# Kernel optimization log

Measured on AMD Instinct MI355X. Metric: run time of the kernel, lower is better.

## Reference

```python
import jax, jax.numpy as jnp
import numpy as np
import math

B, T, D_MOTION = 2, 1536, 256
D_MODEL, N_HEADS, D_FF, N_LAYERS = 512, 8, 2048, 6
D_HEAD = D_MODEL // N_HEADS
FPS = 30
PERIOD = FPS // 2
CONTEXT_FRAMES = 10
NEG = -1e9  # large negative instead of -inf so fully-masked rows give uniform attn, not NaN


def _w(k, shape, fan_in):
    return jax.random.normal(k, shape, jnp.float32) / np.sqrt(fan_in)


def setup_inputs() -> dict:
    key = jax.random.key(0)
    ks = jax.random.split(key, 16)
    L = N_LAYERS
    din = D_MOTION + 5 + 1
    inp = {
        'motion': jax.random.normal(ks[0], (B, T, D_MOTION), jnp.float32),
        'traj': jax.random.normal(ks[1], (B, T, 5), jnp.float32),
        'me_w1': _w(ks[2], (din, D_MODEL), din), 'me_b1': jnp.zeros((D_MODEL,), jnp.float32),
        'me_w2': _w(ks[3], (D_MODEL, D_MODEL), D_MODEL), 'me_b2': jnp.zeros((D_MODEL,), jnp.float32),
        'wq': _w(ks[4], (L, D_MODEL, D_MODEL), D_MODEL), 'bq': jnp.zeros((L, D_MODEL), jnp.float32),
        'wk': _w(ks[5], (L, D_MODEL, D_MODEL), D_MODEL), 'bk': jnp.zeros((L, D_MODEL), jnp.float32),
        'wv': _w(ks[6], (L, D_MODEL, D_MODEL), D_MODEL), 'bv': jnp.zeros((L, D_MODEL), jnp.float32),
        'wo': _w(ks[7], (L, D_MODEL, D_MODEL), D_MODEL), 'bo': jnp.zeros((L, D_MODEL), jnp.float32),
        'ln1_g': jnp.ones((L, D_MODEL), jnp.float32), 'ln1_b': jnp.zeros((L, D_MODEL), jnp.float32),
        'ffn_w1': _w(ks[8], (L, D_MODEL, D_FF), D_MODEL), 'ffn_b1': jnp.zeros((L, D_FF), jnp.float32),
        'ffn_w2': _w(ks[9], (L, D_FF, D_MODEL), D_FF), 'ffn_b2': jnp.zeros((L, D_MODEL), jnp.float32),
        'ln2_g': jnp.ones((L, D_MODEL), jnp.float32), 'ln2_b': jnp.zeros((L, D_MODEL), jnp.float32),
        'fln_g': jnp.ones((D_MODEL,), jnp.float32), 'fln_b': jnp.zeros((D_MODEL,), jnp.float32),
        'dec_w1': _w(ks[10], (D_MODEL, D_MODEL), D_MODEL), 'dec_b1': jnp.zeros((D_MODEL,), jnp.float32),
        'dec_w2': _w(ks[11], (D_MODEL, D_MOTION), D_MODEL), 'dec_b2': jnp.zeros((D_MOTION,), jnp.float32),
    }
    return inp


def _layer_norm(x, g, b):
    m = jnp.mean(x, axis=-1, keepdims=True)
    v = jnp.mean((x - m) ** 2, axis=-1, keepdims=True)
    return (x - m) * jax.lax.rsqrt(v + 1e-5) * g + b


def _leaky(x):
    return jnp.where(x >= 0, x, 0.01 * x)


def _forward(motion, traj, me_w1, me_b1, me_w2, me_b2, wq, bq, wk, bk, wv, bv, wo, bo,
             ln1_g, ln1_b, ffn_w1, ffn_b1, ffn_w2, ffn_b2, ln2_g, ln2_b,
             fln_g, fln_b, dec_w1, dec_b1, dec_w2, dec_b2):
    idx = jnp.arange(T)
    dist = jnp.abs(idx[:, None] - idx[None, :])                       # [T,T]
    atten_bias = -(dist // PERIOD).astype(jnp.float32)                # periodic distance bias

    # context mask: keep first context_frames and last frame
    batch_mask = jnp.ones((T, 1), jnp.float32).at[CONTEXT_FRAMES:-1].set(0.0)
    mask = jnp.broadcast_to(batch_mask[None], (B, T, 1))              # [B,T,1]
    cf = jnp.ones((T,), bool).at[CONTEXT_FRAMES:-1].set(False)        # constrained frames

    original_motion = motion
    motion = motion * mask

    # motion encoder (dropout inactive at eval)
    h = jnp.concatenate([motion, traj, mask], axis=-1)                # [B,T,D_MOTION+6]
    x = _leaky(h @ me_w1 + me_b1)
    x = _leaky(x @ me_w2 + me_b2)

    # periodic positional embedding (sinusoidal on pos mod period)
    pos = jnp.mod(jnp.arange(T, dtype=jnp.float32), float(PERIOD))
    half = D_MODEL // 2
    div = jnp.exp(-np.log(10000.0) * (2.0 * jnp.arange(half, dtype=jnp.float32)) / D_MODEL)
    ang = pos[:, None] * div[None, :]
    pe = jnp.concatenate([jnp.sin(ang), jnp.cos(ang)], axis=-1)       # [T,D_MODEL]
    x = x + pe[None]

    # dynamically growing attention window
    num_trans = T - CONTEXT_FRAMES - 1
    ksz = math.ceil(num_trans / 2 / N_LAYERS) * 2 + 1
    kern = jnp.ones((ksz,), jnp.float32)
    thr = ksz // 2
    scale = 1.0 / np.sqrt(D_HEAD)

    for i in range(N_LAYERS):
        # attn mask: True = blocked
        amask = (dist > thr) | (~cf)[None, :]                         # [T,T]
        h = _layer_norm(x, ln1_g[i], ln1_b[i])                        # pre-layernorm
        q = (h @ wq[i] + bq[i]).reshape(B, T, N_HEADS, D_HEAD)
        k = (h @ wk[i] + bk[i]).reshape(B, T, N_HEADS, D_HEAD)
        v = (h @ wv[i] + bv[i]).reshape(B, T, N_HEADS, D_HEAD)
        scores = jnp.einsum('bqhd,bkhd->bhqk', q, k) * scale + atten_bias
        scores = jnp.where(amask[None, None], NEG, scores)
        attn = jax.nn.softmax(scores, axis=-1)
        out = jnp.einsum('bhqk,bkhd->bqhd', attn, v).reshape(B, T, D_MODEL)
        x = x + out @ wo[i] + bo[i]
        # position-wise FFN (pre-layernorm)
        h = _layer_norm(x, ln2_g[i], ln2_b[i])
        x = x + jax.nn.relu(h @ ffn_w1[i] + ffn_b1[i]) @ ffn_w2[i] + ffn_b2[i]
        # grow constrained frames by conv1d with ones kernel (same padding)
        cf = jnp.convolve(cf.astype(jnp.float32), kern, mode='same') > 0.5

    x = _layer_norm(x, fln_g, fln_b)
    x = _leaky(x @ dec_w1 + dec_b1)
    x = x @ dec_w2 + dec_b2                                           # [B,T,D_MOTION]
    out = original_motion * mask + x * (1.0 - mask)
    return out, mask


def reference(motion, traj, me_w1, me_b1, me_w2, me_b2, wq, bq, wk, bk, wv, bv, wo, bo,
              ln1_g, ln1_b, ffn_w1, ffn_b1, ffn_w2, ffn_b2, ln2_g, ln2_b,
              fln_g, fln_b, dec_w1, dec_b1, dec_w2, dec_b2):
    return _forward(motion, traj, me_w1, me_b1, me_w2, me_b2, wq, bq, wk, bk, wv, bv, wo, bo,
                    ln1_g, ln1_b, ffn_w1, ffn_b1, ffn_w2, ffn_b2, ln2_g, ln2_b,
                    fln_g, fln_b, dec_w1, dec_b1, dec_w2, dec_b2)
```

## Files before the change

kernel.cpp:

```cpp
#include <hip/hip_runtime.h>
#include <math.h>

typedef unsigned short ushort_t;
typedef unsigned int uint_t;
typedef __bf16 bf16x4 __attribute__((ext_vector_type(4)));
typedef __bf16 bf16x8 __attribute__((ext_vector_type(8)));
typedef float f32x4 __attribute__((ext_vector_type(4)));

#define T_SEQ   1536
#define NB      2
#define MROWS   3072
#define DMODEL  512
#define NHEADS  8
#define DHEAD   64
#define DFF     2048
#define DMOTION 256
#define NLAYERS 6
#define PERIODN 15
#define CTXF    10
#define THRW    128
#define KIN     384

__device__ __forceinline__ float bf2f(ushort_t u) { return __uint_as_float((uint_t)u << 16); }
__device__ __forceinline__ ushort_t f2bf(float f) {
    uint_t x = __float_as_uint(f);
    return (ushort_t)((x + 0x7fffu + ((x >> 16) & 1u)) >> 16);
}

__device__ __forceinline__ void gl2lds(const ushort_t* g, ushort_t* l) {
    __builtin_amdgcn_global_load_lds((const __attribute__((address_space(1))) void*)g,
                                     (__attribute__((address_space(3))) void*)l, 16, 0, 0);
}

__global__ __launch_bounds__(256) void pe_k(float* __restrict__ pe) {
    int idx = blockIdx.x * 256 + threadIdx.x;
    if (idx >= PERIODN * DMODEL) return;
    int p = idx / DMODEL, c = idx % DMODEL;
    int j = (c < DMODEL / 2) ? c : (c - DMODEL / 2);
    float div = __expf(-logf(10000.0f) * (2.0f * (float)j) / (float)DMODEL);
    float ang = (float)p * div;
    pe[idx] = (c < DMODEL / 2) ? sinf(ang) : cosf(ang);
}

__global__ __launch_bounds__(256) void build_k(const float* __restrict__ motion,
                                               const float* __restrict__ traj,
                                               ushort_t* __restrict__ hin,
                                               float* __restrict__ mask_out) {
    int idx = blockIdx.x * 256 + threadIdx.x;
    if (idx >= MROWS * KIN) return;
    int row = idx / KIN, c = idx % KIN;
    int t = row % T_SEQ;
    float mv = (t < CTXF || t == T_SEQ - 1) ? 1.0f : 0.0f;
    float val;
    if (c < DMOTION)            val = motion[(size_t)row * DMOTION + c] * mv;
    else if (c < DMOTION + 5)   val = traj[(size_t)row * 5 + (c - DMOTION)];
    else if (c == DMOTION + 5)  val = mv;
    else                        val = 0.0f;
    hin[idx] = f2bf(val);
    if (c == 0) mask_out[row] = mv;
}

__global__ __launch_bounds__(256)
void tconv_k(const float* __restrict__ src, size_t sstride,
             ushort_t* __restrict__ dst, size_t dstride,
             int K, int N, int Kpad) {
    __shared__ float t[32][33];
    src += (size_t)blockIdx.z * sstride;
    dst += (size_t)blockIdx.z * dstride;
    const int kb = blockIdx.y * 32, nb = blockIdx.x * 32;
    const int tx = threadIdx.x & 31, ty = threadIdx.x >> 5;
#pragma unroll
    for (int i = 0; i < 4; ++i) {
        int k = kb + ty + i * 8, n = nb + tx;
        t[ty + i * 8][tx] = (k < K && n < N) ? src[(size_t)k * N + n] : 0.0f;
    }
    __syncthreads();
#pragma unroll
    for (int i = 0; i < 4; ++i) {
        int n = nb + ty + i * 8, kk = kb + tx;
        if (n < N && kk < Kpad) dst[(size_t)n * Kpad + kk] = f2bf(t[tx][ty + i * 8]);
    }
}

__global__ __launch_bounds__(256)
void tconv_qkv_k(const float* __restrict__ wq, const float* __restrict__ wk,
                 const float* __restrict__ wv, ushort_t* __restrict__ qkvt) {
    __shared__ float t[32][33];
    const int z = blockIdx.z, s = z % 3, l = z / 3;
    const float* src = (s == 0 ? wq : s == 1 ? wk : wv) + (size_t)l * DMODEL * DMODEL;
    ushort_t* dst = qkvt + (size_t)z * DMODEL * DMODEL;
    const int kb = blockIdx.y * 32, nb = blockIdx.x * 32;
    const int tx = threadIdx.x & 31, ty = threadIdx.x >> 5;
#pragma unroll
    for (int i = 0; i < 4; ++i)
        t[ty + i * 8][tx] = src[(size_t)(kb + ty + i * 8) * DMODEL + nb + tx];
    __syncthreads();
#pragma unroll
    for (int i = 0; i < 4; ++i)
        dst[(size_t)(nb + ty + i * 8) * DMODEL + kb + tx] = f2bf(t[tx][ty + i * 8]);
}

__global__ __launch_bounds__(256)
void bcat_k(const float* __restrict__ bq, const float* __restrict__ bk,
            const float* __restrict__ bv, float* __restrict__ bqkv) {
    int idx = blockIdx.x * 256 + threadIdx.x;
    if (idx >= NLAYERS * 3 * DMODEL) return;
    int l = idx / (3 * DMODEL), n = idx % (3 * DMODEL);
    int s = n >> 9, c = n & 511;
    const float* b = (s == 0 ? bq : s == 1 ? bk : bv);
    bqkv[idx] = b[l * DMODEL + c];
}

#define CL  68
template <int ACT, bool RES, bool PE, bool OUTBF>
__global__ __launch_bounds__(256)
void qgemm_k(const ushort_t* __restrict__ A, int K,
             const ushort_t* __restrict__ Wt,
             const float* __restrict__ bias,
             const float* __restrict__ res,
             const float* __restrict__ pe15,
             void* __restrict__ Cout, int N) {
    __shared__ ushort_t smem[2][(32 + 64) * 128];
    const int tid = threadIdx.x;
    const int lane = tid & 63, wid = tid >> 6;
    const int m0 = blockIdx.y * 32, n0 = blockIdx.x * 64;
    const int l4 = lane >> 4, l15 = lane & 15;
    const int lrow = lane >> 4;
    const int lu   = lane & 15;

    f32x4 acc[2][4];
#pragma unroll
    for (int m = 0; m < 2; ++m)
#pragma unroll
        for (int n = 0; n < 4; ++n) acc[m][n] = (f32x4){0.f, 0.f, 0.f, 0.f};

    const int niter = K >> 7;

    auto stage = [&](int buf, int k0) {
        ushort_t* dst = &smem[buf][0];
#pragma unroll
        for (int j = 0; j < 6; ++j) {
            const int inst = wid * 6 + j;
            if (inst < 8) {
                const int row = inst * 4 + lrow;
                const int u = lu ^ (row & 15);
                gl2lds(A + (size_t)(m0 + row) * K + k0 + u * 8, dst + inst * 512);
            } else {
                const int bi = inst - 8;
                const int row = bi * 4 + lrow;
                const int u = lu ^ (row & 15);
                gl2lds(Wt + (size_t)(n0 + row) * K + k0 + u * 8,
                       dst + 32 * 128 + bi * 512);
            }
        }
    };

    const int kbyte = wid * 64;
    auto rdfrag = [&](const ushort_t* t, int row) -> bf16x8 {
        const int off0 = kbyte + l4 * 8;
        const int off1 = kbyte + 32 + l4 * 8;
        const int a0 = row * 256 + (((off0 & ~15) ^ ((row & 15) << 4)) | (off0 & 15));
        const int a1 = row * 256 + (((off1 & ~15) ^ ((row & 15) << 4)) | (off1 & 15));
        bf16x4 lo = *(const bf16x4*)((const char*)t + a0);
        bf16x4 hi = *(const bf16x4*)((const char*)t + a1);
        return __builtin_shufflevector(lo, hi, 0, 1, 2, 3, 4, 5, 6, 7);
    };

    stage(0, 0);
    __syncthreads();
    int cur = 0;
    for (int t = 0; t < niter; ++t) {
        if (t + 1 < niter) stage(cur ^ 1, (t + 1) << 7);
        const ushort_t* As = &smem[cur][0];
        const ushort_t* Bs = &smem[cur][32 * 128];
        bf16x8 af[2], bf[4];
#pragma unroll
        for (int m = 0; m < 2; ++m) af[m] = rdfrag(As, m * 16 + l15);
#pragma unroll
        for (int n = 0; n < 4; ++n) bf[n] = rdfrag(Bs, n * 16 + l15);
#pragma unroll
        for (int m = 0; m < 2; ++m)
#pragma unroll
            for (int n = 0; n < 4; ++n)
                acc[m][n] = __builtin_amdgcn_mfma_f32_16x16x32_bf16(af[m], bf[n], acc[m][n], 0, 0, 0);
        __syncthreads();
        cur ^= 1;
    }

    float* cb0 = (float*)&smem[0][0];
    float* cb1 = (float*)&smem[1][0];
    if (wid >= 2) {
        float* cb = (wid == 2) ? cb0 : cb1;
#pragma unroll
        for (int m = 0; m < 2; ++m)
#pragma unroll
            for (int n = 0; n < 4; ++n)
#pragma unroll
                for (int r = 0; r < 4; ++r)
                    cb[(m * 16 + l4 * 4 + r) * CL + n * 16 + l15] = acc[m][n][r];
    }
    __syncthreads();
    if (wid < 2) {
        float* cb = (wid == 0) ? cb0 : cb1;
#pragma unroll
        for (int m = 0; m < 2; ++m)
#pragma unroll
            for (int n = 0; n < 4; ++n)
#pragma unroll
                for (int r = 0; r < 4; ++r)
                    cb[(m * 16 + l4 * 4 + r) * CL + n * 16 + l15] += acc[m][n][r];
    }
    __syncthreads();

    const int row = tid >> 3, c0 = (tid & 7) * 8;
    const int grow = m0 + row;
#pragma unroll
    for (int j = 0; j < 8; ++j) {
        const int gcol = n0 + c0 + j;
        float v = cb0[row * CL + c0 + j] + cb1[row * CL + c0 + j] + bias[gcol];
        if (ACT == 1) v = v >= 0.f ? v : 0.01f * v;
        else if (ACT == 2) v = fmaxf(v, 0.f);
        else if (ACT == 3) {
            const int t2 = grow % T_SEQ;
            const float mv = (t2 < CTXF || t2 == T_SEQ - 1) ? 1.0f : 0.0f;
            v = res[(size_t)grow * N + gcol] * mv + v * (1.0f - mv);
        }
        if (PE) v += pe15[((grow % T_SEQ) % PERIODN) * DMODEL + gcol];
        if (RES) v += res[(size_t)grow * N + gcol];
        if (OUTBF) ((ushort_t*)Cout)[(size_t)grow * N + gcol] = f2bf(v);
        else       ((float*)Cout)[(size_t)grow * N + gcol] = v;
    }
}

template <bool RES, bool OUTBF>
__global__ __launch_bounds__(256)
void pgemm_k(const ushort_t* __restrict__ A,
             const ushort_t* __restrict__ Wt,
             const float* __restrict__ bias,
             const float* __restrict__ res,
             void* __restrict__ Cout, int ldc,
             int tpb, int len1, int start2, int nact) {
    __shared__ ushort_t smem[2][(32 + 64) * 128];
    const int tid = threadIdx.x;
    const int lane = tid & 63, wid = tid >> 6;
    const int ty = blockIdx.y;
    const int bb = (ty >= tpb) ? 1 : 0;
    const int t32 = (ty - bb * tpb) * 32;
    const int n0 = blockIdx.x * 64;
    const int l4 = lane >> 4, l15 = lane & 15;
    const int lrow = lane >> 4;
    const int lu   = lane & 15;

    auto maprow = [&](int pr) -> size_t {
        int r = t32 + pr;
        r = min(r, nact - 1);
        int tt = (r < len1) ? r : (start2 + (r - len1));
        return (size_t)(bb * T_SEQ + tt);
    };

    f32x4 acc[2][4];
#pragma unroll
    for (int m = 0; m < 2; ++m)
#pragma unroll
        for (int n = 0; n < 4; ++n) acc[m][n] = (f32x4){0.f, 0.f, 0.f, 0.f};

    auto stage = [&](int buf, int k0) {
        ushort_t* dst = &smem[buf][0];
#pragma unroll
        for (int j = 0; j < 6; ++j) {
            const int inst = wid * 6 + j;
            if (inst < 8) {
                const int row = inst * 4 + lrow;
                const int u = lu ^ (row & 15);
                gl2lds(A + maprow(row) * 512 + k0 + u * 8, dst + inst * 512);
            } else {
                const int bi = inst - 8;
                const int row = bi * 4 + lrow;
                const int u = lu ^ (row & 15);
                gl2lds(Wt + (size_t)(n0 + row) * 512 + k0 + u * 8,
                       dst + 32 * 128 + bi * 512);
            }
        }
    };

    const int kbyte = wid * 64;
    auto rdfrag = [&](const ushort_t* t, int row) -> bf16x8 {
        const int off0 = kbyte + l4 * 8;
        const int off1 = kbyte + 32 + l4 * 8;
        const int a0 = row * 256 + (((off0 & ~15) ^ ((row & 15) << 4)) | (off0 & 15));
        const int a1 = row * 256 + (((off1 & ~15) ^ ((row & 15) << 4)) | (off1 & 15));
        bf16x4 lo = *(const bf16x4*)((const char*)t + a0);
        bf16x4 hi = *(const bf16x4*)((const char*)t + a1);
        return __builtin_shufflevector(lo, hi, 0, 1, 2, 3, 4, 5, 6, 7);
    };

    stage(0, 0);
    __syncthreads();
    int cur = 0;
    for (int t = 0; t < 4; ++t) {
        if (t + 1 < 4) stage(cur ^ 1, (t + 1) << 7);
        const ushort_t* As = &smem[cur][0];
        const ushort_t* Bs = &smem[cur][32 * 128];
        bf16x8 af[2], bf[4];
#pragma unroll
        for (int m = 0; m < 2; ++m) af[m] = rdfrag(As, m * 16 + l15);
#pragma unroll
        for (int n = 0; n < 4; ++n) bf[n] = rdfrag(Bs, n * 16 + l15);
#pragma unroll
        for (int m = 0; m < 2; ++m)
#pragma unroll
            for (int n = 0; n < 4; ++n)
                acc[m][n] = __builtin_amdgcn_mfma_f32_16x16x32_bf16(af[m], bf[n], acc[m][n], 0, 0, 0);
        __syncthreads();
        cur ^= 1;
    }

    float* cb0 = (float*)&smem[0][0];
    float* cb1 = (float*)&smem[1][0];
    if (wid >= 2) {
        float* cb = (wid == 2) ? cb0 : cb1;
#pragma unroll
        for (int m = 0; m < 2; ++m)
#pragma unroll
            for (int n = 0; n < 4; ++n)
#pragma unroll
                for (int r = 0; r < 4; ++r)
                    cb[(m * 16 + l4 * 4 + r) * CL + n * 16 + l15] = acc[m][n][r];
    }
    __syncthreads();
    if (wid < 2) {
        float* cb = (wid == 0) ? cb0 : cb1;
#pragma unroll
        for (int m = 0; m < 2; ++m)
#pragma unroll
            for (int n = 0; n < 4; ++n)
#pragma unroll
                for (int r = 0; r < 4; ++r)
                    cb[(m * 16 + l4 * 4 + r) * CL + n * 16 + l15] += acc[m][n][r];
    }
    __syncthreads();

    const int row = tid >> 3, c0 = (tid & 7) * 8;
    const int pr = t32 + row;
    if (pr >= nact) return;
    const int tt = (pr < len1) ? pr : (start2 + (pr - len1));
    const size_t grow = (size_t)(bb * T_SEQ + tt);
#pragma unroll
    for (int j = 0; j < 8; ++j) {
        const int gcol = n0 + c0 + j;
        float v = cb0[row * CL + c0 + j] + cb1[row * CL + c0 + j] + bias[gcol];
        if (RES) v += res[grow * ldc + gcol];
        if (OUTBF) ((ushort_t*)Cout)[grow * ldc + gcol] = f2bf(v);
        else       ((float*)Cout)[grow * ldc + gcol] = v;
    }
}

__global__ __launch_bounds__(256)
void ln_k(const float* __restrict__ X, const float* __restrict__ g,
          const float* __restrict__ b, ushort_t* __restrict__ Y) {
    const int wid = threadIdx.x >> 6, lane = threadIdx.x & 63;
    const int row = blockIdx.x * 4 + wid;
    const float* x = X + (size_t)row * DMODEL;
    float v[8], s = 0.f;
#pragma unroll
    for (int j = 0; j < 8; ++j) { v[j] = x[lane + 64 * j]; s += v[j]; }
#pragma unroll
    for (int o = 32; o; o >>= 1) s += __shfl_xor(s, o);
    const float mean = s * (1.0f / DMODEL);
    float vs = 0.f;
#pragma unroll
    for (int j = 0; j < 8; ++j) { float d = v[j] - mean; vs += d * d; }
#pragma unroll
    for (int o = 32; o; o >>= 1) vs += __shfl_xor(vs, o);
    const float inv = rsqrtf(vs * (1.0f / DMODEL) + 1e-5f);
    ushort_t* y = Y + (size_t)row * DMODEL;
#pragma unroll
    for (int j = 0; j < 8; ++j) {
        const int c = lane + 64 * j;
        y[c] = f2bf((v[j] - mean) * inv * g[c] + b[c]);
    }
}

__global__ __launch_bounds__(1024)
void vsum_k(const ushort_t* __restrict__ h, float* __restrict__ hp) {
    __shared__ float red[16][512];
    const int b = blockIdx.x, ch = blockIdx.y;
    const int rg = threadIdx.x >> 6;
    const int c8 = (threadIdx.x & 63) * 8;
    const ushort_t* hb = h + (size_t)(b * T_SEQ + ch * 192) * DMODEL + c8;
    float a[8] = {};
    for (int r = rg; r < 192; r += 16) {
        bf16x8 v = *(const bf16x8*)(hb + (size_t)r * DMODEL);
#pragma unroll
        for (int j = 0; j < 8; ++j) a[j] += (float)v[j];
    }
#pragma unroll
    for (int j = 0; j < 8; ++j) red[rg][c8 + j] = a[j];
    __syncthreads();
    if (threadIdx.x < 512) {
        float s = 0.f;
#pragma unroll
        for (int gi = 0; gi < 16; ++gi) s += red[gi][threadIdx.x];
        hp[(b * 8 + ch) * 512 + threadIdx.x] = s;
    }
}

__global__ __launch_bounds__(256)
void vdot_k(const float* __restrict__ hp, const ushort_t* __restrict__ wvt,
            const float* __restrict__ bv, float* __restrict__ vm) {
    __shared__ float mh[512];
    __shared__ float red[256];
    const int b = blockIdx.x, seg = blockIdx.y;
    const int t = threadIdx.x;
    for (int c = t; c < 512; c += 256) {
        float s = 0.f;
#pragma unroll
        for (int ch = 0; ch < 8; ++ch) s += hp[(b * 8 + ch) * 512 + c];
        mh[c] = s * (1.0f / T_SEQ);
    }
    __syncthreads();
    const int col = seg * 128 + (t & 127);
    const int kh = (t >> 7) * 256;
    const ushort_t* w = wvt + (size_t)col * 512 + kh;
    float s = 0.f;
    for (int k = 0; k < 256; k += 8) {
        bf16x8 w8 = *(const bf16x8*)(w + k);
#pragma unroll
        for (int j = 0; j < 8; ++j) s += mh[kh + k + j] * (float)w8[j];
    }
    red[t] = s;
    __syncthreads();
    if (t < 128) vm[b * 512 + col] = red[t] + red[t + 128] + bv[col];
}

__global__ __launch_bounds__(256)
void gemv_k(const float* __restrict__ vin, const ushort_t* __restrict__ wt,
            const float* __restrict__ bias, float* __restrict__ vout) {
    __shared__ float mh[512];
    __shared__ float red[256];
    const int b = blockIdx.x, seg = blockIdx.y;
    const int t = threadIdx.x;
    for (int c = t; c < 512; c += 256) mh[c] = vin[b * 512 + c];
    __syncthreads();
    const int col = seg * 128 + (t & 127);
    const int kh = (t >> 7) * 256;
    const ushort_t* w = wt + (size_t)col * 512 + kh;
    float s = 0.f;
    for (int k = 0; k < 256; k += 8) {
        bf16x8 w8 = *(const bf16x8*)(w + k);
#pragma unroll
        for (int j = 0; j < 8; ++j) s += mh[kh + k + j] * (float)w8[j];
    }
    red[t] = s;
    __syncthreads();
    if (t < 128) vout[b * 512 + col] = red[t] + red[t + 128] + bias[col];
}

__global__ __launch_bounds__(256)
void xadd_k(const float* __restrict__ vmo, float* __restrict__ x, int q0) {
    const int row = q0 + blockIdx.x, b = blockIdx.y;
    float* xr = x + (size_t)(b * T_SEQ + row) * DMODEL;
    const float* vb = vmo + b * 512;
    xr[threadIdx.x]       += vb[threadIdx.x];
    xr[threadIdx.x + 256] += vb[threadIdx.x + 256];
}

#define KLD 72
#define VLD 36
__global__ __launch_bounds__(256)
void attn3_k(const ushort_t* __restrict__ qkv, ushort_t* __restrict__ attout,
             int lo, int hi, int nlow, int qhi0, int tl, int st) {
    __shared__ ushort_t klds_[4][32 * KLD];
    __shared__ ushort_t vlds_[4][64 * VLD];
    const int lane = threadIdx.x & 63, wid = threadIdx.x >> 6;
    const int s = blockIdx.x * 4 + wid;
    if (s >= st) return;
    const int h = blockIdx.y, b = blockIdx.z;
    const int l15 = lane & 15, l4 = lane >> 4;

    int qb, qend;
    if (s < tl) { qb = 16 * s;                qend = nlow - 1; }
    else        { qb = qhi0 + 16 * (s - tl);  qend = T_SEQ - 1; }
    const int nr = qend - qb;

    ushort_t* klds = klds_[wid];
    ushort_t* vlds = vlds_[wid];
    const size_t rbase = (size_t)(b * T_SEQ) * 1536;
    const int q = qb + l15;

    const int qrow_r = min(q, T_SEQ - 1);
    const ushort_t* qptr = qkv + rbase + (size_t)qrow_r * 1536 + h * 64;
    bf16x8 bq[2];
#pragma unroll
    for (int kh = 0; kh < 2; ++kh) {
        bf16x4 lo4 = *(const bf16x4*)(qptr + kh * 32 + l4 * 4);
        bf16x4 hi4 = *(const bf16x4*)(qptr + kh * 32 + 16 + l4 * 4);
        bq[kh] = __builtin_shufflevector(lo4, hi4, 0, 1, 2, 3, 4, 5, 6, 7);
    }

    const int band0 = max(0, qb - THRW);
    const int band1 = min(T_SEQ - 1, qb + 15 + THRW);
    const int i1s = band0, i1e = min(band1, lo - 1);
    const int i2s = max(band0, hi), i2e = band1;

    f32x4 O[4] = {{0.f,0.f,0.f,0.f},{0.f,0.f,0.f,0.f},{0.f,0.f,0.f,0.f},{0.f,0.f,0.f,0.f}};
    float m = -3.0e38f, lsum = 0.f;

#pragma unroll 1
    for (int seg = 0; seg < 2; ++seg) {
        const int s0 = seg ? i2s : i1s, s1 = seg ? i2e : i1e;
#pragma unroll 1
        for (int c0 = s0; c0 <= s1; c0 += 32) {
#pragma unroll
            for (int i = 0; i < 4; ++i) {
                const int idx = i * 64 + lane;
                const int row = idx >> 3, c = (idx & 7) * 8;
                const int kr = min(c0 + row, T_SEQ - 1);
                const uint4 kv = *(const uint4*)(qkv + rbase + (size_t)kr * 1536 + 512 + h * 64 + c);
                *(uint4*)&klds[row * KLD + c] = kv;
                const uint4 vv = *(const uint4*)(qkv + rbase + (size_t)kr * 1536 + 1024 + h * 64 + c);
                const ushort_t* vp = (const ushort_t*)&vv;
#pragma unroll
                for (int d = 0; d < 8; ++d) vlds[(c + d) * VLD + row] = vp[d];
            }
            f32x4 sacc[2];
#pragma unroll
            for (int ks = 0; ks < 2; ++ks) {
                f32x4 a = {0.f, 0.f, 0.f, 0.f};
#pragma unroll
                for (int kh = 0; kh < 2; ++kh) {
                    const ushort_t* kp = &klds[(16 * ks + l15) * KLD + kh * 32];
                    bf16x4 lo4 = *(const bf16x4*)(kp + l4 * 4);
                    bf16x4 hi4 = *(const bf16x4*)(kp + 16 + l4 * 4);
                    bf16x8 ak = __builtin_shufflevector(lo4, hi4, 0, 1, 2, 3, 4, 5, 6, 7);
                    a = __builtin_amdgcn_mfma_f32_16x16x32_bf16(ak, bq[kh], a, 0, 0, 0);
                }
                sacc[ks] = a;
            }
            float sv[8];
            bool vld[8];
            float cm = -3.0e38f;
#pragma unroll
            for (int ks = 0; ks < 2; ++ks)
#pragma unroll
                for (int r = 0; r < 4; ++r) {
                    const int key = c0 + 16 * ks + 4 * l4 + r;
                    const int dist = (q > key) ? (q - key) : (key - q);
                    const bool v = (dist <= THRW) && (key < lo || key >= hi) && (key < T_SEQ);
                    const int ii = ks * 4 + r;
                    sv[ii] = sacc[ks][r] * 0.125f - (float)(dist / PERIODN);
                    vld[ii] = v;
                    cm = fmaxf(cm, v ? sv[ii] : -3.0e38f);
                }
            cm = fmaxf(cm, __shfl_xor(cm, 16));
            cm = fmaxf(cm, __shfl_xor(cm, 32));
            const float mnew = fmaxf(m, cm);
            const float sc = __expf(m - mnew);
            m = mnew;
            float p[8], psum = 0.f;
#pragma unroll
            for (int ii = 0; ii < 8; ++ii) {
                p[ii] = vld[ii] ? __expf(sv[ii] - mnew) : 0.f;
                psum += p[ii];
            }
            psum += __shfl_xor(psum, 16);
            psum += __shfl_xor(psum, 32);
            lsum = lsum * sc + psum;
#pragma unroll
            for (int ds = 0; ds < 4; ++ds) O[ds] *= sc;
            bf16x8 pb;
#pragma unroll
            for (int ii = 0; ii < 8; ++ii) pb[ii] = (__bf16)p[ii];
#pragma unroll
            for (int ds = 0; ds < 4; ++ds) {
                const ushort_t* vp2 = &vlds[(16 * ds + l15) * VLD];
                bf16x4 lo4 = *(const bf16x4*)(vp2 + 4 * l4);
                bf16x4 hi4 = *(const bf16x4*)(vp2 + 16 + 4 * l4);
                bf16x8 av = __builtin_shufflevector(lo4, hi4, 0, 1, 2, 3, 4, 5, 6, 7);
                O[ds] = __builtin_amdgcn_mfma_f32_16x16x32_bf16(av, pb, O[ds], 0, 0, 0);
            }
        }
    }
    if (l15 <= nr) {
        const float inv = 1.0f / lsum;
        ushort_t* op = attout + (size_t)(b * T_SEQ + qb + l15) * DMODEL + h * 64;
#pragma unroll
        for (int ds = 0; ds < 4; ++ds)
#pragma unroll
            for (int r = 0; r < 4; ++r)
                op[16 * ds + 4 * l4 + r] = f2bf(O[ds][r] * inv);
    }
}

extern "C" void kernel_launch(void* const* d_in, const int* in_sizes, int n_in,
                              void* d_out, int out_size, void* d_ws, size_t ws_size,
                              hipStream_t stream) {
    const float* motion = (const float*)d_in[0];
    const float* traj   = (const float*)d_in[1];
    const float* me_w1  = (const float*)d_in[2];
    const float* me_b1  = (const float*)d_in[3];
    const float* me_w2  = (const float*)d_in[4];
    const float* me_b2  = (const float*)d_in[5];
    const float* wq = (const float*)d_in[6];
    const float* bq = (const float*)d_in[7];
    const float* wk = (const float*)d_in[8];
    const float* bk = (const float*)d_in[9];
    const float* wv = (const float*)d_in[10];
    const float* bv = (const float*)d_in[11];
    const float* wo = (const float*)d_in[12];
    const float* bo = (const float*)d_in[13];
    const float* ln1_g = (const float*)d_in[14];
    const float* ln1_b = (const float*)d_in[15];
    const float* ffn_w1 = (const float*)d_in[16];
    const float* ffn_b1 = (const float*)d_in[17];
    const float* ffn_w2 = (const float*)d_in[18];
    const float* ffn_b2 = (const float*)d_in[19];
    const float* ln2_g = (const float*)d_in[20];
    const float* ln2_b = (const float*)d_in[21];
    const float* fln_g = (const float*)d_in[22];
    const float* fln_b = (const float*)d_in[23];
    const float* dec_w1 = (const float*)d_in[24];
    const float* dec_b1 = (const float*)d_in[25];
    const float* dec_w2 = (const float*)d_in[26];
    const float* dec_b2 = (const float*)d_in[27];

    float* out = (float*)d_out;
    float* mask_out = out + (size_t)MROWS * DMOTION;

    char* base = (char*)d_ws;
    auto alloc = [&](size_t bytes) { char* p = base; base += (bytes + 255) & ~(size_t)255; return p; };

    ushort_t* qkvt  = (ushort_t*)alloc((size_t)NLAYERS * 1536 * 512 * 2);
    ushort_t* wot   = (ushort_t*)alloc((size_t)NLAYERS * 512 * 512 * 2);
    ushort_t* ffn1t = (ushort_t*)alloc((size_t)NLAYERS * 2048 * 512 * 2);
    ushort_t* ffn2t = (ushort_t*)alloc((size_t)NLAYERS * 512 * 2048 * 2);
    ushort_t* mew1t = (ushort_t*)alloc((size_t)512 * KIN * 2);
    ushort_t* mew2t = (ushort_t*)alloc((size_t)512 * 512 * 2);
    ushort_t* dec1t = (ushort_t*)alloc((size_t)512 * 512 * 2);
    ushort_t* dec2t = (ushort_t*)alloc((size_t)256 * 512 * 2);
    float*    bqkv  = (float*)alloc((size_t)NLAYERS * 1536 * 4);
    float*    pe15  = (float*)alloc((size_t)PERIODN * DMODEL * 4);
    float*    hp    = (float*)alloc((size_t)NB * 8 * 512 * 4);
    float*    vm    = (float*)alloc((size_t)NB * 512 * 4);
    float*    vmo   = (float*)alloc((size_t)NB * 512 * 4);
    ushort_t* hin   = (ushort_t*)alloc((size_t)MROWS * KIN * 2);
    float*    x     = (float*)alloc((size_t)MROWS * DMODEL * 4);
    ushort_t* h     = (ushort_t*)alloc((size_t)MROWS * DMODEL * 2);
    ushort_t* qkv   = (ushort_t*)alloc((size_t)MROWS * 1536 * 2);
    ushort_t* ff    = (ushort_t*)alloc((size_t)MROWS * DFF * 2);

    const dim3 blk(256);
    pe_k<<<(PERIODN * DMODEL + 255) / 256, blk, 0, stream>>>(pe15);
    build_k<<<(MROWS * KIN + 255) / 256, blk, 0, stream>>>(motion, traj, hin, mask_out);

    tconv_qkv_k<<<dim3(16, 16, 18), blk, 0, stream>>>(wq, wk, wv, qkvt);
    tconv_k<<<dim3(16, 16, 6), blk, 0, stream>>>(wo, 512 * 512, wot, 512 * 512, 512, 512, 512);
    tconv_k<<<dim3(64, 16, 6), blk, 0, stream>>>(ffn_w1, 512 * 2048, ffn1t, 2048 * 512, 512, 2048, 512);
    tconv_k<<<dim3(16, 64, 6), blk, 0, stream>>>(ffn_w2, 2048 * 512, ffn2t, 512 * 2048, 2048, 512, 2048);
    tconv_k<<<dim3(16, 12, 1), blk, 0, stream>>>(me_w1, 0, mew1t, 0, 262, 512, KIN);
    tconv_k<<<dim3(16, 16, 1), blk, 0, stream>>>(me_w2, 0, mew2t, 0, 512, 512, 512);
    tconv_k<<<dim3(16, 16, 1), blk, 0, stream>>>(dec_w1, 0, dec1t, 0, 512, 512, 512);
    tconv_k<<<dim3(8, 16, 1),  blk, 0, stream>>>(dec_w2, 0, dec2t, 0, 512, 256, 512);
    bcat_k<<<(NLAYERS * 1536 + 255) / 256, blk, 0, stream>>>(bq, bk, bv, bqkv);

    const dim3 gs512(8, 96), gsff(32, 96), gs256(4, 96);

    qgemm_k<1, false, false, true ><<<gs512, blk, 0, stream>>>(hin, KIN, mew1t, me_b1, nullptr, nullptr, h, 512);
    qgemm_k<1, false, true,  false><<<gs512, blk, 0, stream>>>(h, 512, mew2t, me_b2, nullptr, pe15, x, 512);

    for (int i = 0; i < NLAYERS; ++i) {
        const int lo = CTXF + THRW * i;
        const int hi = (T_SEQ - 1) - THRW * i;
        int qlow_end = lo + 127;
        int qhi0 = hi - 128;
        int nlow, ninact;
        if (qhi0 <= qlow_end + 1) {
            nlow = T_SEQ; qhi0 = T_SEQ; ninact = 0;
        } else {
            nlow = qlow_end + 1;
            ninact = qhi0 - nlow;
        }
        const int tl2 = (nlow + 15) / 16;
        const int th2 = (T_SEQ - qhi0 + 15) / 16;
        const int st  = tl2 + th2;
        const int nact_q = nlow + (T_SEQ - qhi0);
        const int tpb_q  = (nact_q + 31) / 32;
        const int nkeys  = lo + (T_SEQ - hi);
        const int tpb_kv = (nkeys + 31) / 32;

        const ushort_t* qw  = qkvt + (size_t)i * 1536 * 512;
        const ushort_t* kvw = qw + (size_t)512 * 512;
        const ushort_t* vw  = qw + (size_t)1024 * 512;
        const float* bq_i   = bqkv + i * 1536;

        ln_k<<<MROWS / 4, blk, 0, stream>>>(x, ln1_g + i * 512, ln1_b + i * 512, h);
        pgemm_k<false, true><<<dim3(8, 2 * tpb_q), blk, 0, stream>>>(
            h, qw, bq_i, nullptr, qkv, 1536, tpb_q, nlow, qhi0, nact_q);
        pgemm_k<false, true><<<dim3(16, 2 * tpb_kv), blk, 0, stream>>>(
            h, kvw, bq_i + 512, nullptr, qkv + 512, 1536, tpb_kv, lo, hi, nkeys);
        if (ninact > 0) {
            vsum_k<<<dim3(NB, 8), dim3(1024), 0, stream>>>(h, hp);
            vdot_k<<<dim3(NB, 4), blk, 0, stream>>>(hp, vw, bq_i + 1024, vm);
            gemv_k<<<dim3(NB, 4), blk, 0, stream>>>(vm, wot + (size_t)i * 512 * 512, bo + i * 512, vmo);
            xadd_k<<<dim3(ninact, NB), blk, 0, stream>>>(vmo, x, nlow);
        }
        attn3_k<<<dim3((st + 3) / 4, NHEADS, NB), blk, 0, stream>>>(qkv, h, lo, hi, nlow, qhi0, tl2, st);
        pgemm_k<true, false><<<dim3(8, 2 * tpb_q), blk, 0, stream>>>(
            h, wot + (size_t)i * 512 * 512, bo + i * 512, x, x, 512, tpb_q, nlow, qhi0, nact_q);
        ln_k<<<MROWS / 4, blk, 0, stream>>>(x, ln2_g + i * 512, ln2_b + i * 512, h);
        qgemm_k<2, false, false, true><<<gsff, blk, 0, stream>>>(h, 512, ffn1t + (size_t)i * 2048 * 512, ffn_b1 + i * 2048, nullptr, nullptr, ff, 2048);
        qgemm_k<0, true, false, false><<<gs512, blk, 0, stream>>>(ff, 2048, ffn2t + (size_t)i * 512 * 2048, ffn_b2 + i * 512, x, nullptr, x, 512);
    }

    ln_k<<<MROWS / 4, blk, 0, stream>>>(x, fln_g, fln_b, h);
    qgemm_k<1, false, false, true ><<<gs512, blk, 0, stream>>>(h, 512, dec1t, dec_b1, nullptr, nullptr, ff, 512);
    qgemm_k<3, false, false, false><<<gs256, blk, 0, stream>>>(ff, 512, dec2t, dec_b2, motion, nullptr, out, 256);
}
```

Before: 831.2 us.

## Merge weight transposes, Q/KV projections, and inactive-row vector path into fewer kernels

All weight transpose-convert launches are collapsed into one flat-grid kernel. The separate Q and KV projection GEMMs are merged into a single qkv_k launch that picks its role from blockIdx. The vdot/gemv pair becomes one 512-thread kernel, and the xadd broadcast into inactive rows is folded into the second layernorm, which adds vmo and writes x back. Together these cut launch count and one pass over x per layer, at the cost of wasted early-exit blocks in qkv_k and a larger serial gemv in a single block per batch.

```diff
diff --git a/kernel.cpp b/kernel.cpp
--- a/kernel.cpp
+++ b/kernel.cpp
@@ -61,13 +61,54 @@
 }
 
 __global__ __launch_bounds__(256)
-void tconv_k(const float* __restrict__ src, size_t sstride,
-             ushort_t* __restrict__ dst, size_t dstride,
-             int K, int N, int Kpad) {
+void tconv_all_k(const float* __restrict__ wq, const float* __restrict__ wk,
+                 const float* __restrict__ wv, const float* __restrict__ wo,
+                 const float* __restrict__ fw1, const float* __restrict__ fw2,
+                 const float* __restrict__ mw1, const float* __restrict__ mw2,
+                 const float* __restrict__ dw1, const float* __restrict__ dw2,
+                 ushort_t* __restrict__ qkvt, ushort_t* __restrict__ wot,
+                 ushort_t* __restrict__ ffn1t, ushort_t* __restrict__ ffn2t,
+                 ushort_t* __restrict__ mew1t, ushort_t* __restrict__ mew2t,
+                 ushort_t* __restrict__ dec1t, ushort_t* __restrict__ dec2t) {
     __shared__ float t[32][33];
-    src += (size_t)blockIdx.z * sstride;
-    dst += (size_t)blockIdx.z * dstride;
-    const int kb = blockIdx.y * 32, nb = blockIdx.x * 32;
+    int bid = blockIdx.x;
+    const float* src; ushort_t* dst;
+    int K, N, Kpad, kb, nb;
+    if (bid < 4608) {
+        int z = bid >> 8, r = bid & 255;
+        int s = z % 3, l = z / 3;
+        src = (s == 0 ? wq : s == 1 ? wk : wv) + (size_t)l * 262144;
+        dst = qkvt + (size_t)z * 262144;
+        K = 512; N = 512; Kpad = 512; kb = (r >> 4) * 32; nb = (r & 15) * 32;
+    } else if (bid < 6144) {
+        int b2 = bid - 4608; int z = b2 >> 8, r = b2 & 255;
+        src = wo + (size_t)z * 262144; dst = wot + (size_t)z * 262144;
+        K = 512; N = 512; Kpad = 512; kb = (r >> 4) * 32; nb = (r & 15) * 32;
+    } else if (bid < 12288) {
+        int b2 = bid - 6144; int z = b2 >> 10, r = b2 & 1023;
+        src = fw1 + (size_t)z * 1048576; dst = ffn1t + (size_t)z * 1048576;
+        K = 512; N = 2048; Kpad = 512; kb = (r >> 6) * 32; nb = (r & 63) * 32;
+    } else if (bid < 18432) {
+        int b2 = bid - 12288; int z = b2 >> 10, r = b2 & 1023;
+        src = fw2 + (size_t)z * 1048576; dst = ffn2t + (size_t)z * 1048576;
+        K = 2048; N = 512; Kpad = 2048; kb = (r >> 4) * 32; nb = (r & 15) * 32;
+    } else if (bid < 18624) {
+        int r = bid - 18432;
+        src = mw1; dst = mew1t;
+        K = 262; N = 512; Kpad = KIN; kb = (r >> 4) * 32; nb = (r & 15) * 32;
+    } else if (bid < 18880) {
+        int r = bid - 18624;
+        src = mw2; dst = mew2t;
+        K = 512; N = 512; Kpad = 512; kb = (r >> 4) * 32; nb = (r & 15) * 32;
+    } else if (bid < 19136) {
+        int r = bid - 18880;
+        src = dw1; dst = dec1t;
+        K = 512; N = 512; Kpad = 512; kb = (r >> 4) * 32; nb = (r & 15) * 32;
+    } else {
+        int r = bid - 19136;
+        src = dw2; dst = dec2t;
+        K = 512; N = 256; Kpad = 512; kb = (r >> 3) * 32; nb = (r & 7) * 32;
+    }
     const int tx = threadIdx.x & 31, ty = threadIdx.x >> 5;
 #pragma unroll
     for (int i = 0; i < 4; ++i) {
@@ -80,24 +121,6 @@
         int n = nb + ty + i * 8, kk = kb + tx;
         if (n < N && kk < Kpad) dst[(size_t)n * Kpad + kk] = f2bf(t[tx][ty + i * 8]);
     }
-}
-
-__global__ __launch_bounds__(256)
-void tconv_qkv_k(const float* __restrict__ wq, const float* __restrict__ wk,
-                 const float* __restrict__ wv, ushort_t* __restrict__ qkvt) {
-    __shared__ float t[32][33];
-    const int z = blockIdx.z, s = z % 3, l = z / 3;
-    const float* src = (s == 0 ? wq : s == 1 ? wk : wv) + (size_t)l * DMODEL * DMODEL;
-    ushort_t* dst = qkvt + (size_t)z * DMODEL * DMODEL;
-    const int kb = blockIdx.y * 32, nb = blockIdx.x * 32;
-    const int tx = threadIdx.x & 31, ty = threadIdx.x >> 5;
-#pragma unroll
-    for (int i = 0; i < 4; ++i)
-        t[ty + i * 8][tx] = src[(size_t)(kb + ty + i * 8) * DMODEL + nb + tx];
-    __syncthreads();
-#pragma unroll
-    for (int i = 0; i < 4; ++i)
-        dst[(size_t)(nb + ty + i * 8) * DMODEL + kb + tx] = f2bf(t[tx][ty + i * 8]);
 }
 
 __global__ __launch_bounds__(256)
@@ -356,6 +379,134 @@
 }
 
 __global__ __launch_bounds__(256)
+void qkv_k(const ushort_t* __restrict__ A,
+           const ushort_t* __restrict__ qw, const ushort_t* __restrict__ kvw,
+           const float* __restrict__ biasq, ushort_t* __restrict__ Cout,
+           int tpbQ, int len1Q, int start2Q, int nactQ,
+           int tpbK, int len1K, int start2K, int nactK) {
+    __shared__ ushort_t smem[2][(32 + 64) * 128];
+    const int tid = threadIdx.x;
+    const int lane = tid & 63, wid = tid >> 6;
+    int tyl, tpb, len1, start2, nact, outoff;
+    const ushort_t* W;
+    if ((int)blockIdx.y < 2 * tpbQ) {
+        if (blockIdx.x >= 8) return;
+        tyl = blockIdx.y; tpb = tpbQ; len1 = len1Q; start2 = start2Q; nact = nactQ;
+        outoff = 0; W = qw;
+    } else {
+        tyl = blockIdx.y - 2 * tpbQ; tpb = tpbK; len1 = len1K; start2 = start2K; nact = nactK;
+        outoff = 512; W = kvw;
+    }
+    const int bb = (tyl >= tpb) ? 1 : 0;
+    const int t32 = (tyl - bb * tpb) * 32;
+    const int n0 = blockIdx.x * 64;
+    const int l4 = lane >> 4, l15 = lane & 15;
+    const int lrow = lane >> 4;
+    const int lu   = lane & 15;
+
+    auto maprow = [&](int pr) -> size_t {
+        int r = t32 + pr;
+        r = min(r, nact - 1);
+        int tt = (r < len1) ? r : (start2 + (r - len1));
+        return (size_t)(bb * T_SEQ + tt);
+    };
+
+    f32x4 acc[2][4];
+#pragma unroll
+    for (int m = 0; m < 2; ++m)
+#pragma unroll
+        for (int n = 0; n < 4; ++n) acc[m][n] = (f32x4){0.f, 0.f, 0.f, 0.f};
+
+    auto stage = [&](int buf, int k0) {
+        ushort_t* dst = &smem[buf][0];
+#pragma unroll
+        for (int j = 0; j < 6; ++j) {
+            const int inst = wid * 6 + j;
+            if (inst < 8) {
+                const int row = inst * 4 + lrow;
+                const int u = lu ^ (row & 15);
+                gl2lds(A + maprow(row) * 512 + k0 + u * 8, dst + inst * 512);
+            } else {
+                const int bi = inst - 8;
+                const int row = bi * 4 + lrow;
+                const int u = lu ^ (row & 15);
+                gl2lds(W + (size_t)(n0 + row) * 512 + k0 + u * 8,
+                       dst + 32 * 128 + bi * 512);
+            }
+        }
+    };
+
+    const int kbyte = wid * 64;
+    auto rdfrag = [&](const ushort_t* t, int row) -> bf16x8 {
+        const int off0 = kbyte + l4 * 8;
+        const int off1 = kbyte + 32 + l4 * 8;
+        const int a0 = row * 256 + (((off0 & ~15) ^ ((row & 15) << 4)) | (off0 & 15));
+        const int a1 = row * 256 + (((off1 & ~15) ^ ((row & 15) << 4)) | (off1 & 15));
+        bf16x4 lo = *(const bf16x4*)((const char*)t + a0);
+        bf16x4 hi = *(const bf16x4*)((const char*)t + a1);
+        return __builtin_shufflevector(lo, hi, 0, 1, 2, 3, 4, 5, 6, 7);
+    };
+
+    stage(0, 0);
+    __syncthreads();
+    int cur = 0;
+    for (int t = 0; t < 4; ++t) {
+        if (t + 1 < 4) stage(cur ^ 1, (t + 1) << 7);
+        const ushort_t* As = &smem[cur][0];
+        const ushort_t* Bs = &smem[cur][32 * 128];
+        bf16x8 af[2], bf[4];
+#pragma unroll
+        for (int m = 0; m < 2; ++m) af[m] = rdfrag(As, m * 16 + l15);
+#pragma unroll
+        for (int n = 0; n < 4; ++n) bf[n] = rdfrag(Bs, n * 16 + l15);
+#pragma unroll
+        for (int m = 0; m < 2; ++m)
+#pragma unroll
+            for (int n = 0; n < 4; ++n)
+                acc[m][n] = __builtin_amdgcn_mfma_f32_16x16x32_bf16(af[m], bf[n], acc[m][n], 0, 0, 0);
+        __syncthreads();
+        cur ^= 1;
+    }
+
+    float* cb0 = (float*)&smem[0][0];
+    float* cb1 = (float*)&smem[1][0];
+    if (wid >= 2) {
+        float* cb = (wid == 2) ? cb0 : cb1;
+#pragma unroll
+        for (int m = 0; m < 2; ++m)
+#pragma unroll
+            for (int n = 0; n < 4; ++n)
+#pragma unroll
+                for (int r = 0; r < 4; ++r)
+                    cb[(m * 16 + l4 * 4 + r) * CL + n * 16 + l15] = acc[m][n][r];
+    }
+    __syncthreads();
+    if (wid < 2) {
+        float* cb = (wid == 0) ? cb0 : cb1;
+#pragma unroll
+        for (int m = 0; m < 2; ++m)
+#pragma unroll
+            for (int n = 0; n < 4; ++n)
+#pragma unroll
+                for (int r = 0; r < 4; ++r)
+                    cb[(m * 16 + l4 * 4 + r) * CL + n * 16 + l15] += acc[m][n][r];
+    }
+    __syncthreads();
+
+    const int row = tid >> 3, c0 = (tid & 7) * 8;
+    const int pr = t32 + row;
+    if (pr >= nact) return;
+    const int tt = (pr < len1) ? pr : (start2 + (pr - len1));
+    const size_t grow = (size_t)(bb * T_SEQ + tt);
+#pragma unroll
+    for (int j = 0; j < 8; ++j) {
+        const int gcol = outoff + n0 + c0 + j;
+        float v = cb0[row * CL + c0 + j] + cb1[row * CL + c0 + j] + biasq[gcol];
+        Cout[grow * 1536 + gcol] = f2bf(v);
+    }
+}
+
+__global__ __launch_bounds__(256)
 void ln_k(const float* __restrict__ X, const float* __restrict__ g,
           const float* __restrict__ b, ushort_t* __restrict__ Y) {
     const int wid = threadIdx.x >> 6, lane = threadIdx.x & 63;
@@ -364,6 +515,43 @@
     float v[8], s = 0.f;
 #pragma unroll
     for (int j = 0; j < 8; ++j) { v[j] = x[lane + 64 * j]; s += v[j]; }
+#pragma unroll
+    for (int o = 32; o; o >>= 1) s += __shfl_xor(s, o);
+    const float mean = s * (1.0f / DMODEL);
+    float vs = 0.f;
+#pragma unroll
+    for (int j = 0; j < 8; ++j) { float d = v[j] - mean; vs += d * d; }
+#pragma unroll
+    for (int o = 32; o; o >>= 1) vs += __shfl_xor(vs, o);
+    const float inv = rsqrtf(vs * (1.0f / DMODEL) + 1e-5f);
+    ushort_t* y = Y + (size_t)row * DMODEL;
+#pragma unroll
+    for (int j = 0; j < 8; ++j) {
+        const int c = lane + 64 * j;
+        y[c] = f2bf((v[j] - mean) * inv * g[c] + b[c]);
+    }
+}
+
+__global__ __launch_bounds__(256)
+void ln2x_k(float* __restrict__ X, const float* __restrict__ vmo,
+            const float* __restrict__ g, const float* __restrict__ b,
+            ushort_t* __restrict__ Y, int iLo, int iHi) {
+    const int wid = threadIdx.x >> 6, lane = threadIdx.x & 63;
+    const int row = blockIdx.x * 4 + wid;
+    const int t = row % T_SEQ, bb = row / T_SEQ;
+    const bool inact = (t >= iLo) && (t < iHi);
+    float* x = X + (size_t)row * DMODEL;
+    float v[8], s = 0.f;
+#pragma unroll
+    for (int j = 0; j < 8; ++j) {
+        const int c = lane + 64 * j;
+        v[j] = x[c] + (inact ? vmo[bb * 512 + c] : 0.f);
+        s += v[j];
+    }
+    if (inact) {
+#pragma unroll
+        for (int j = 0; j < 8; ++j) x[lane + 64 * j] = v[j];
+    }
 #pragma unroll
     for (int o = 32; o; o >>= 1) s += __shfl_xor(s, o);
     const float mean = s * (1.0f / DMODEL);
@@ -405,64 +593,35 @@
     }
 }
 
-__global__ __launch_bounds__(256)
-void vdot_k(const float* __restrict__ hp, const ushort_t* __restrict__ wvt,
-            const float* __restrict__ bv, float* __restrict__ vm) {
+__global__ __launch_bounds__(512)
+void vmg_k(const float* __restrict__ hp, const ushort_t* __restrict__ wvt,
+           const float* __restrict__ bv, const ushort_t* __restrict__ wot_l,
+           const float* __restrict__ bo_l, float* __restrict__ vmo) {
     __shared__ float mh[512];
-    __shared__ float red[256];
-    const int b = blockIdx.x, seg = blockIdx.y;
-    const int t = threadIdx.x;
-    for (int c = t; c < 512; c += 256) {
-        float s = 0.f;
-#pragma unroll
-        for (int ch = 0; ch < 8; ++ch) s += hp[(b * 8 + ch) * 512 + c];
-        mh[c] = s * (1.0f / T_SEQ);
-    }
-    __syncthreads();
-    const int col = seg * 128 + (t & 127);
-    const int kh = (t >> 7) * 256;
-    const ushort_t* w = wvt + (size_t)col * 512 + kh;
+    __shared__ float vmld[512];
+    const int b = blockIdx.x, t = threadIdx.x;
     float s = 0.f;
-    for (int k = 0; k < 256; k += 8) {
+#pragma unroll
+    for (int ch = 0; ch < 8; ++ch) s += hp[(b * 8 + ch) * 512 + t];
+    mh[t] = s * (1.0f / T_SEQ);
+    __syncthreads();
+    const ushort_t* w = wvt + (size_t)t * 512;
+    float acc = 0.f;
+    for (int k = 0; k < 512; k += 8) {
         bf16x8 w8 = *(const bf16x8*)(w + k);
 #pragma unroll
-        for (int j = 0; j < 8; ++j) s += mh[kh + k + j] * (float)w8[j];
-    }
-    red[t] = s;
-    __syncthreads();
-    if (t < 128) vm[b * 512 + col] = red[t] + red[t + 128] + bv[col];
-}
-
-__global__ __launch_bounds__(256)
-void gemv_k(const float* __restrict__ vin, const ushort_t* __restrict__ wt,
-            const float* __restrict__ bias, float* __restrict__ vout) {
-    __shared__ float mh[512];
-    __shared__ float red[256];
-    const int b = blockIdx.x, seg = blockIdx.y;
-    const int t = threadIdx.x;
-    for (int c = t; c < 512; c += 256) mh[c] = vin[b * 512 + c];
-    __syncthreads();
-    const int col = seg * 128 + (t & 127);
-    const int kh = (t >> 7) * 256;
-    const ushort_t* w = wt + (size_t)col * 512 + kh;
-    float s = 0.f;
-    for (int k = 0; k < 256; k += 8) {
-        bf16x8 w8 = *(const bf16x8*)(w + k);
-#pragma unroll
-        for (int j = 0; j < 8; ++j) s += mh[kh + k + j] * (float)w8[j];
-    }
-    red[t] = s;
-    __syncthreads();
-    if (t < 128) vout[b * 512 + col] = red[t] + red[t + 128] + bias[col];
-}
-
-__global__ __launch_bounds__(256)
-void xadd_k(const float* __restrict__ vmo, float* __restrict__ x, int q0) {
-    const int row = q0 + blockIdx.x, b = blockIdx.y;
-    float* xr = x + (size_t)(b * T_SEQ + row) * DMODEL;
-    const float* vb = vmo + b * 512;
-    xr[threadIdx.x]       += vb[threadIdx.x];
-    xr[threadIdx.x + 256] += vb[threadIdx.x + 256];
+        for (int j = 0; j < 8; ++j) acc += mh[k + j] * (float)w8[j];
+    }
+    vmld[t] = acc + bv[t];
+    __syncthreads();
+    const ushort_t* w2 = wot_l + (size_t)t * 512;
+    acc = 0.f;
+    for (int k = 0; k < 512; k += 8) {
+        bf16x8 w8 = *(const bf16x8*)(w2 + k);
+#pragma unroll
+        for (int j = 0; j < 8; ++j) acc += vmld[k + j] * (float)w8[j];
+    }
+    vmo[b * 512 + t] = acc + bo_l[t];
 }
 
 #define KLD 72
@@ -641,7 +800,6 @@
     float*    bqkv  = (float*)alloc((size_t)NLAYERS * 1536 * 4);
     float*    pe15  = (float*)alloc((size_t)PERIODN * DMODEL * 4);
     float*    hp    = (float*)alloc((size_t)NB * 8 * 512 * 4);
-    float*    vm    = (float*)alloc((size_t)NB * 512 * 4);
     float*    vmo   = (float*)alloc((size_t)NB * 512 * 4);
     ushort_t* hin   = (ushort_t*)alloc((size_t)MROWS * KIN * 2);
     float*    x     = (float*)alloc((size_t)MROWS * DMODEL * 4);
@@ -652,15 +810,10 @@
     const dim3 blk(256);
     pe_k<<<(PERIODN * DMODEL + 255) / 256, blk, 0, stream>>>(pe15);
     build_k<<<(MROWS * KIN + 255) / 256, blk, 0, stream>>>(motion, traj, hin, mask_out);
-
-    tconv_qkv_k<<<dim3(16, 16, 18), blk, 0, stream>>>(wq, wk, wv, qkvt);
-    tconv_k<<<dim3(16, 16, 6), blk, 0, stream>>>(wo, 512 * 512, wot, 512 * 512, 512, 512, 512);
-    tconv_k<<<dim3(64, 16, 6), blk, 0, stream>>>(ffn_w1, 512 * 2048, ffn1t, 2048 * 512, 512, 2048, 512);
-    tconv_k<<<dim3(16, 64, 6), blk, 0, stream>>>(ffn_w2, 2048 * 512, ffn2t, 512 * 2048, 2048, 512, 2048);
-    tconv_k<<<dim3(16, 12, 1), blk, 0, stream>>>(me_w1, 0, mew1t, 0, 262, 512, KIN);
-    tconv_k<<<dim3(16, 16, 1), blk, 0, stream>>>(me_w2, 0, mew2t, 0, 512, 512, 512);
-    tconv_k<<<dim3(16, 16, 1), blk, 0, stream>>>(dec_w1, 0, dec1t, 0, 512, 512, 512);
-    tconv_k<<<dim3(8, 16, 1),  blk, 0, stream>>>(dec_w2, 0, dec2t, 0, 512, 256, 512);
+    tconv_all_k<<<19264, blk, 0, stream>>>(wq, wk, wv, wo, ffn_w1, ffn_w2,
+                                           me_w1, me_w2, dec_w1, dec_w2,
+                                           qkvt, wot, ffn1t, ffn2t,
+                                           mew1t, mew2t, dec1t, dec2t);
     bcat_k<<<(NLAYERS * 1536 + 255) / 256, blk, 0, stream>>>(bq, bk, bv, bqkv);
 
     const dim3 gs512(8, 96), gsff(32, 96), gs256(4, 96);
@@ -692,22 +845,21 @@
         const ushort_t* kvw = qw + (size_t)512 * 512;
         const ushort_t* vw  = qw + (size_t)1024 * 512;
         const float* bq_i   = bqkv + i * 1536;
+        const ushort_t* wot_i = wot + (size_t)i * 512 * 512;
 
         ln_k<<<MROWS / 4, blk, 0, stream>>>(x, ln1_g + i * 512, ln1_b + i * 512, h);
-        pgemm_k<false, true><<<dim3(8, 2 * tpb_q), blk, 0, stream>>>(
-            h, qw, bq_i, nullptr, qkv, 1536, tpb_q, nlow, qhi0, nact_q);
-        pgemm_k<false, true><<<dim3(16, 2 * tpb_kv), blk, 0, stream>>>(
-            h, kvw, bq_i + 512, nullptr, qkv + 512, 1536, tpb_kv, lo, hi, nkeys);
+        qkv_k<<<dim3(16, 2 * tpb_q + 2 * tpb_kv), blk, 0, stream>>>(
+            h, qw, kvw, bq_i, qkv,
+            tpb_q, nlow, qhi0, nact_q, tpb_kv, lo, hi, nkeys);
         if (ninact > 0) {
             vsum_k<<<dim3(NB, 8), dim3(1024), 0, stream>>>(h, hp);
-            vdot_k<<<dim3(NB, 4), blk, 0, stream>>>(hp, vw, bq_i + 1024, vm);
-            gemv_k<<<dim3(NB, 4), blk, 0, stream>>>(vm, wot + (size_t)i * 512 * 512, bo + i * 512, vmo);
-            xadd_k<<<dim3(ninact, NB), blk, 0, stream>>>(vmo, x, nlow);
+            vmg_k<<<dim3(NB), dim3(512), 0, stream>>>(hp, vw, bq_i + 1024, wot_i, bo + i * 512, vmo);
         }
         attn3_k<<<dim3((st + 3) / 4, NHEADS, NB), blk, 0, stream>>>(qkv, h, lo, hi, nlow, qhi0, tl2, st);
         pgemm_k<true, false><<<dim3(8, 2 * tpb_q), blk, 0, stream>>>(
-            h, wot + (size_t)i * 512 * 512, bo + i * 512, x, x, 512, tpb_q, nlow, qhi0, nact_q);
-        ln_k<<<MROWS / 4, blk, 0, stream>>>(x, ln2_g + i * 512, ln2_b + i * 512, h);
+            h, wot_i, bo + i * 512, x, x, 512, tpb_q, nlow, qhi0, nact_q);
+        ln2x_k<<<MROWS / 4, blk, 0, stream>>>(x, vmo, ln2_g + i * 512, ln2_b + i * 512, h,
+                                              ninact > 0 ? nlow : 0, ninact > 0 ? qhi0 : 0);
         qgemm_k<2, false, false, true><<<gsff, blk, 0, stream>>>(h, 512, ffn1t + (size_t)i * 2048 * 512, ffn_b1 + i * 2048, nullptr, nullptr, ff, 2048);
         qgemm_k<0, true, false, false><<<gs512, blk, 0, stream>>>(ff, 2048, ffn2t + (size_t)i * 512 * 2048, ffn_b2 + i * 512, x, nullptr, x, 512);
     }
```

Measured after the change: 892.3 us. +7.4%, slower.
